# Kernel optimization log

Hardware: AMD Instinct MI355X
Metric: run time of the kernel (lower is better)

Reference implementation:

```python
import jax, jax.numpy as jnp
import numpy as np

N_USERS = 1_000_000
AVG_DEG = 32
E = N_USERS * AVG_DEG
K = 5
IN_F = 1
OUT_F = 64
BN_EPS = 1e-5


def setup_inputs() -> dict:
    key = jax.random.key(0)
    ks = jax.random.split(key, 6)
    stdv = 1.0 / np.sqrt(IN_F * K)
    return {
        "x": jax.random.normal(ks[0], (N_USERS, IN_F), dtype=jnp.float32),
        "edge_index": jax.random.randint(ks[1], (2, E), 0, N_USERS, dtype=jnp.int32),
        "edge_weight": jax.random.uniform(ks[2], (E,), dtype=jnp.float32),
        "weight": jax.random.uniform(ks[3], (OUT_F, K, IN_F), dtype=jnp.float32, minval=-stdv, maxval=stdv),
        "bias": jax.random.uniform(ks[4], (OUT_F,), dtype=jnp.float32, minval=-stdv, maxval=stdv),
        "gamma": jnp.ones((N_USERS,), dtype=jnp.float32),
        "beta": jnp.zeros((N_USERS,), dtype=jnp.float32),
    }


def reference(x, edge_index, edge_weight, weight, bias, gamma, beta):
    N = x.shape[0]
    src, dst = edge_index[0], edge_index[1]
    # K-hop propagation: gather x_j, scale by edge_weight, scatter-add at dst
    feats = [x]
    cur = x
    for _ in range(K - 1):
        msg = cur[src] * edge_weight[:, None]                 # [E, IN_F]
        cur = jax.ops.segment_sum(msg, dst, num_segments=N)   # [N, IN_F]
        feats.append(cur)
    # [N, K*IN_F], hop-major / feature-minor ordering (matches torch reshape)
    conv = jnp.concatenate(feats, axis=1)[None]               # [1, N, K*IN_F]
    h = weight.reshape(OUT_F, K * IN_F).T                     # [K*IN_F, OUT_F]
    y = jnp.matmul(conv, h) + bias                            # [1, N, OUT_F]
    # BatchNorm1d(N_users) in training mode: stats over (batch, feature) per node-channel
    mean = jnp.mean(y, axis=(0, 2), keepdims=True)
    var = jnp.mean((y - mean) ** 2, axis=(0, 2), keepdims=True)  # biased var
    y_hat = (y - mean) * jax.lax.rsqrt(var + BN_EPS)
    return y_hat * gamma[None, :, None] + beta[None, :, None]
```

## Files before the change

### kernel.cpp

```cpp
#include <hip/hip_runtime.h>

#define N_USERS 1000000
#define NEDGE   32000000
#define OUT_F   64
#define BN_EPS  1e-5f

#define SBITS     12
#define S_BUCKET  4096
#define NB        245
#define CAP       136896
#define SCAT_BLOCKS 1024
#define TILE      4096
#define NTILES    ((NEDGE + TILE - 1) / TILE)
#define SPLIT     8

typedef unsigned int uint4v __attribute__((ext_vector_type(4)));


__global__ void init_cursors(unsigned* __restrict__ cursors) {
    int i = blockIdx.x * blockDim.x + threadIdx.x;
    if (i < NB) cursors[i] = (unsigned)i * CAP;
}

__global__ __launch_bounds__(256) void scatter_bin(
    const int* __restrict__ src, const int* __restrict__ dst,
    const float* __restrict__ ew, uint2* __restrict__ rec,
    unsigned* __restrict__ cursors) {
    __shared__ uint2 srec[TILE];
    __shared__ unsigned short sbkt[TILE];
    __shared__ unsigned hist[NB];
    __shared__ unsigned curs[NB];
    __shared__ unsigned gpos[NB];
    int tid = threadIdx.x;

    for (int tile = blockIdx.x; tile < NTILES; tile += gridDim.x) {
        int e0 = tile * TILE;
        int n_this = (e0 + TILE <= NEDGE) ? TILE : (NEDGE - e0);

        for (int i = tid; i < NB; i += 256) hist[i] = 0;
        __syncthreads();

        int d[16];
        #pragma unroll
        for (int k = 0; k < 16; ++k) {
            int e = e0 + k * 256 + tid;
            if (e < NEDGE) {
                d[k] = __builtin_nontemporal_load(&dst[e]);
                atomicAdd(&hist[d[k] >> SBITS], 1u);
            }
        }
        __syncthreads();

        if (tid == 0) {
            unsigned run = 0;
            for (int b = 0; b < NB; ++b) { unsigned v = hist[b]; hist[b] = run; run += v; }
        }
        __syncthreads();

        for (int b = tid; b < NB; b += 256) {
            unsigned st = hist[b];
            unsigned en = (b == NB - 1) ? (unsigned)n_this : hist[b + 1];
            unsigned c = en - st;
            gpos[b] = c ? atomicAdd(&cursors[b], c) : 0u;
            curs[b] = 0;
        }
        __syncthreads();

        #pragma unroll
        for (int k = 0; k < 16; ++k) {
            int e = e0 + k * 256 + tid;
            if (e < NEDGE) {
                int dd = d[k];
                int b = dd >> SBITS;
                int s = __builtin_nontemporal_load(&src[e]);
                float w = __builtin_nontemporal_load(&ew[e]);
                unsigned p = hist[b] + atomicAdd(&curs[b], 1u);
                srec[p] = make_uint2(((unsigned)(dd & (S_BUCKET - 1)) << 20) | (unsigned)s,
                                     __float_as_uint(w));
                sbkt[p] = (unsigned short)b;
            }
        }
        __syncthreads();

        for (int i = tid; i < n_this; i += 256) {
            unsigned b = sbkt[i];
            rec[gpos[b] + ((unsigned)i - hist[b])] = srec[i];
        }
        __syncthreads();
    }
}

__global__ __launch_bounds__(256) void hop_bucket(
    const uint2* __restrict__ rec, const unsigned* __restrict__ cursors,
    const float* __restrict__ cur, float* __restrict__ nxt) {
    __shared__ float acc[S_BUCKET];
    int tid = threadIdx.x;
    int b = blockIdx.x / SPLIT;
    int sidx = blockIdx.x % SPLIT;
    for (int i = tid; i < S_BUCKET; i += 256) acc[i] = 0.0f;
    __syncthreads();

    unsigned start = (unsigned)b * CAP;
    unsigned cnt = cursors[b] - start;
    unsigned u0 = ((cnt * (unsigned)sidx) / SPLIT) & ~3u;
    unsigned u1 = (sidx == SPLIT - 1) ? cnt : (((cnt * (unsigned)(sidx + 1)) / SPLIT) & ~3u);
    const uint2* bp = rec + start;

    unsigned i = u0 + 4u * (unsigned)tid;
    for (; i + 4u <= u1; i += 4u * 256u) {
        uint4v r0 = __builtin_nontemporal_load(reinterpret_cast<const uint4v*>(bp + i));
        uint4v r1 = __builtin_nontemporal_load(reinterpret_cast<const uint4v*>(bp + i + 2));
        float c0 = cur[r0.x & 0xFFFFFu];
        float c1 = cur[r0.z & 0xFFFFFu];
        float c2 = cur[r1.x & 0xFFFFFu];
        float c3 = cur[r1.z & 0xFFFFFu];
        atomicAdd(&acc[r0.x >> 20], c0 * __uint_as_float(r0.y));
        atomicAdd(&acc[r0.z >> 20], c1 * __uint_as_float(r0.w));
        atomicAdd(&acc[r1.x >> 20], c2 * __uint_as_float(r1.y));
        atomicAdd(&acc[r1.z >> 20], c3 * __uint_as_float(r1.w));
    }
    if (i < u1) {
        for (unsigned j = i; j < i + 4u && j < u1; ++j) {
            uint2 r = bp[j];
            atomicAdd(&acc[r.x >> 20], cur[r.x & 0xFFFFFu] * __uint_as_float(r.y));
        }
    }
    __syncthreads();

    int nb0 = b << SBITS;
    for (int k = tid; k < S_BUCKET; k += 256) {
        int n = nb0 + k;
        if (n < N_USERS) atomicAdd(&nxt[n], acc[k]);
    }
}


__global__ void zero_kernel(float* __restrict__ p, int n) {
    int i = blockIdx.x * blockDim.x + threadIdx.x;
    int stride = gridDim.x * blockDim.x;
    for (; i < n; i += stride) p[i] = 0.0f;
}

__global__ __launch_bounds__(256) void hop_atomic(
    const int* __restrict__ src, const int* __restrict__ dst,
    const float* __restrict__ ew, const float* __restrict__ cur,
    float* __restrict__ nxt) {
    int e = blockIdx.x * blockDim.x + threadIdx.x;
    if (e * 4 < NEDGE) {
        int4   s = ((const int4*)src)[e];
        int4   d = ((const int4*)dst)[e];
        float4 w = ((const float4*)ew)[e];
        atomicAdd(&nxt[d.x], cur[s.x] * w.x);
        atomicAdd(&nxt[d.y], cur[s.y] * w.y);
        atomicAdd(&nxt[d.z], cur[s.z] * w.z);
        atomicAdd(&nxt[d.w], cur[s.w] * w.w);
    }
}


__global__ __launch_bounds__(256) void finalize_kernel(
    const float* __restrict__ x,  const float* __restrict__ f1,
    const float* __restrict__ f2, const float* __restrict__ f3,
    const float* __restrict__ f4, const float* __restrict__ W,
    const float* __restrict__ bias, const float* __restrict__ gamma,
    const float* __restrict__ beta, float* __restrict__ out) {
    int lane = threadIdx.x & 63;
    int waveInBlock = threadIdx.x >> 6;
    int wavesPerBlock = blockDim.x >> 6;
    int gwave  = blockIdx.x * wavesPerBlock + waveInBlock;
    int nwaves = gridDim.x * wavesPerBlock;

    float w0 = W[lane * 5 + 0];
    float w1 = W[lane * 5 + 1];
    float w2 = W[lane * 5 + 2];
    float w3 = W[lane * 5 + 3];
    float w4 = W[lane * 5 + 4];
    float b  = bias[lane];

    for (int n = gwave; n < N_USERS; n += nwaves) {
        float c0 = x[n], c1 = f1[n], c2 = f2[n], c3 = f3[n], c4 = f4[n];
        float y = b + c0 * w0 + c1 * w1 + c2 * w2 + c3 * w3 + c4 * w4;

        float s = y;
        #pragma unroll
        for (int off = 32; off; off >>= 1) s += __shfl_xor(s, off);
        float mean = s * (1.0f / 64.0f);

        float d = y - mean;
        float v = d * d;
        #pragma unroll
        for (int off = 32; off; off >>= 1) v += __shfl_xor(v, off);
        float var = v * (1.0f / 64.0f);

        float o = d * rsqrtf(var + BN_EPS) * gamma[n] + beta[n];
        __builtin_nontemporal_store(o, &out[(size_t)n * OUT_F + lane]);
    }
}

extern "C" void kernel_launch(void* const* d_in, const int* in_sizes, int n_in,
                              void* d_out, int out_size, void* d_ws, size_t ws_size,
                              hipStream_t stream) {
    const float* x     = (const float*)d_in[0];
    const int*   ei    = (const int*)d_in[1];
    const float* ew    = (const float*)d_in[2];
    const float* W     = (const float*)d_in[3];
    const float* bias  = (const float*)d_in[4];
    const float* gamma = (const float*)d_in[5];
    const float* beta  = (const float*)d_in[6];
    float* out = (float*)d_out;

    const int* src = ei;
    const int* dst = ei + NEDGE;

    float* f = (float*)d_ws;
    uint2* rec = (uint2*)(f + 4ull * N_USERS);
    unsigned* cursors = (unsigned*)(rec + (size_t)NB * CAP);
    size_t needed = 16000000ull + (size_t)NB * CAP * 8 + 4096;

    if (ws_size >= needed) {
        init_cursors<<<1, 256, 0, stream>>>(cursors);
        zero_kernel<<<2048, 256, 0, stream>>>(f, 4 * N_USERS);
        scatter_bin<<<SCAT_BLOCKS, 256, 0, stream>>>(src, dst, ew, rec, cursors);
        const float* cur = x;
        for (int h = 0; h < 4; ++h) {
            float* nxt = f + (size_t)h * N_USERS;
            hop_bucket<<<NB * SPLIT, 256, 0, stream>>>(rec, cursors, cur, nxt);
            cur = nxt;
        }
    } else {
        zero_kernel<<<4096, 256, 0, stream>>>(f, 4 * N_USERS);
        const float* cur = x;
        for (int h = 0; h < 4; ++h) {
            float* nxt = f + (size_t)h * N_USERS;
            hop_atomic<<<NEDGE / 4 / 256, 256, 0, stream>>>(src, dst, ew, cur, nxt);
            cur = nxt;
        }
    }

    finalize_kernel<<<2048, 256, 0, stream>>>(
        x, f, f + N_USERS, f + 2 * N_USERS, f + 3 * N_USERS,
        W, bias, gamma, beta, out);
}
```

Before: 1.781 ms.

## Sub-bin destination buckets by source quarter to localize gathers

Each destination bucket is split into four sub-bins by which quarter of the source-node range the edge reads from. Each hop block then walks the sub-bins in order, so at any moment the blocks gather from a narrower slice of the feature array, aiming for better L2 locality. The serial prefix scan in the binning kernel becomes a two-level parallel scan to cope with four times as many bins. Costs include more global cursors and atomics, more load imbalance because the per-bin capacity is tighter, and more loop overhead per hop block.

```diff
diff --git a/kernel.cpp b/kernel.cpp
--- a/kernel.cpp
+++ b/kernel.cpp
@@ -8,7 +8,10 @@
 #define SBITS     12
 #define S_BUCKET  4096
 #define NB        245
-#define CAP       136896
+#define KSRC      4
+#define QW        250000
+#define NBINS     (NB * KSRC)
+#define CAP_BIN   34832
 #define SCAT_BLOCKS 1024
 #define TILE      4096
 #define NTILES    ((NEDGE + TILE - 1) / TILE)
@@ -16,10 +19,14 @@
 
 typedef unsigned int uint4v __attribute__((ext_vector_type(4)));
 
+__device__ __forceinline__ int src_quarter(unsigned s) {
+    return (s >= 1u * QW) + (s >= 2u * QW) + (s >= 3u * QW);
+}
+
 
 __global__ void init_cursors(unsigned* __restrict__ cursors) {
     int i = blockIdx.x * blockDim.x + threadIdx.x;
-    if (i < NB) cursors[i] = (unsigned)i * CAP;
+    if (i < NBINS) cursors[i] = (unsigned)i * CAP_BIN;
 }
 
 __global__ __launch_bounds__(256) void scatter_bin(
@@ -28,41 +35,67 @@
     unsigned* __restrict__ cursors) {
     __shared__ uint2 srec[TILE];
     __shared__ unsigned short sbkt[TILE];
-    __shared__ unsigned hist[NB];
-    __shared__ unsigned curs[NB];
-    __shared__ unsigned gpos[NB];
+    __shared__ unsigned hist[NBINS];
+    __shared__ unsigned curs[NBINS];
+    __shared__ unsigned gpos[NBINS];
+    __shared__ unsigned chunkT[256];
     int tid = threadIdx.x;
 
     for (int tile = blockIdx.x; tile < NTILES; tile += gridDim.x) {
         int e0 = tile * TILE;
         int n_this = (e0 + TILE <= NEDGE) ? TILE : (NEDGE - e0);
 
-        for (int i = tid; i < NB; i += 256) hist[i] = 0;
-        __syncthreads();
-
-        int d[16];
+        for (int i = tid; i < NBINS; i += 256) hist[i] = 0;
+        __syncthreads();
+
+        int dv[16], sv[16];
         #pragma unroll
         for (int k = 0; k < 16; ++k) {
             int e = e0 + k * 256 + tid;
             if (e < NEDGE) {
-                d[k] = __builtin_nontemporal_load(&dst[e]);
-                atomicAdd(&hist[d[k] >> SBITS], 1u);
-            }
-        }
-        __syncthreads();
-
+                dv[k] = __builtin_nontemporal_load(&dst[e]);
+                sv[k] = __builtin_nontemporal_load(&src[e]);
+                int bin = ((dv[k] >> SBITS) << 2) | src_quarter((unsigned)sv[k]);
+                atomicAdd(&hist[bin], 1u);
+            }
+        }
+        __syncthreads();
+
+        {
+            int base = tid * 4;
+            unsigned run = 0;
+            #pragma unroll
+            for (int k = 0; k < 4; ++k) {
+                int idx = base + k;
+                unsigned v = (idx < NBINS) ? hist[idx] : 0u;
+                if (idx < NBINS) hist[idx] = run;
+                run += v;
+            }
+            chunkT[tid] = run;
+        }
+        __syncthreads();
         if (tid == 0) {
-            unsigned run = 0;
-            for (int b = 0; b < NB; ++b) { unsigned v = hist[b]; hist[b] = run; run += v; }
-        }
-        __syncthreads();
-
-        for (int b = tid; b < NB; b += 256) {
-            unsigned st = hist[b];
-            unsigned en = (b == NB - 1) ? (unsigned)n_this : hist[b + 1];
+            unsigned r = 0;
+            for (int t = 0; t < 256; ++t) { unsigned v = chunkT[t]; chunkT[t] = r; r += v; }
+        }
+        __syncthreads();
+        {
+            int base = tid * 4;
+            unsigned add = chunkT[tid];
+            #pragma unroll
+            for (int k = 0; k < 4; ++k) {
+                int idx = base + k;
+                if (idx < NBINS) hist[idx] += add;
+            }
+        }
+        __syncthreads();
+
+        for (int bn = tid; bn < NBINS; bn += 256) {
+            unsigned st = hist[bn];
+            unsigned en = (bn == NBINS - 1) ? (unsigned)n_this : hist[bn + 1];
             unsigned c = en - st;
-            gpos[b] = c ? atomicAdd(&cursors[b], c) : 0u;
-            curs[b] = 0;
+            gpos[bn] = c ? atomicAdd(&cursors[bn], c) : 0u;
+            curs[bn] = 0;
         }
         __syncthreads();
 
@@ -70,21 +103,20 @@
         for (int k = 0; k < 16; ++k) {
             int e = e0 + k * 256 + tid;
             if (e < NEDGE) {
-                int dd = d[k];
-                int b = dd >> SBITS;
-                int s = __builtin_nontemporal_load(&src[e]);
+                int dd = dv[k], ss = sv[k];
+                int bin = ((dd >> SBITS) << 2) | src_quarter((unsigned)ss);
                 float w = __builtin_nontemporal_load(&ew[e]);
-                unsigned p = hist[b] + atomicAdd(&curs[b], 1u);
-                srec[p] = make_uint2(((unsigned)(dd & (S_BUCKET - 1)) << 20) | (unsigned)s,
+                unsigned p = hist[bin] + atomicAdd(&curs[bin], 1u);
+                srec[p] = make_uint2(((unsigned)(dd & (S_BUCKET - 1)) << 20) | (unsigned)ss,
                                      __float_as_uint(w));
-                sbkt[p] = (unsigned short)b;
+                sbkt[p] = (unsigned short)bin;
             }
         }
         __syncthreads();
 
         for (int i = tid; i < n_this; i += 256) {
-            unsigned b = sbkt[i];
-            rec[gpos[b] + ((unsigned)i - hist[b])] = srec[i];
+            unsigned bn = sbkt[i];
+            rec[gpos[bn] + ((unsigned)i - hist[bn])] = srec[i];
         }
         __syncthreads();
     }
@@ -100,29 +132,32 @@
     for (int i = tid; i < S_BUCKET; i += 256) acc[i] = 0.0f;
     __syncthreads();
 
-    unsigned start = (unsigned)b * CAP;
-    unsigned cnt = cursors[b] - start;
-    unsigned u0 = ((cnt * (unsigned)sidx) / SPLIT) & ~3u;
-    unsigned u1 = (sidx == SPLIT - 1) ? cnt : (((cnt * (unsigned)(sidx + 1)) / SPLIT) & ~3u);
-    const uint2* bp = rec + start;
-
-    unsigned i = u0 + 4u * (unsigned)tid;
-    for (; i + 4u <= u1; i += 4u * 256u) {
-        uint4v r0 = __builtin_nontemporal_load(reinterpret_cast<const uint4v*>(bp + i));
-        uint4v r1 = __builtin_nontemporal_load(reinterpret_cast<const uint4v*>(bp + i + 2));
-        float c0 = cur[r0.x & 0xFFFFFu];
-        float c1 = cur[r0.z & 0xFFFFFu];
-        float c2 = cur[r1.x & 0xFFFFFu];
-        float c3 = cur[r1.z & 0xFFFFFu];
-        atomicAdd(&acc[r0.x >> 20], c0 * __uint_as_float(r0.y));
-        atomicAdd(&acc[r0.z >> 20], c1 * __uint_as_float(r0.w));
-        atomicAdd(&acc[r1.x >> 20], c2 * __uint_as_float(r1.y));
-        atomicAdd(&acc[r1.z >> 20], c3 * __uint_as_float(r1.w));
-    }
-    if (i < u1) {
-        for (unsigned j = i; j < i + 4u && j < u1; ++j) {
-            uint2 r = bp[j];
-            atomicAdd(&acc[r.x >> 20], cur[r.x & 0xFFFFFu] * __uint_as_float(r.y));
+    for (int k = 0; k < KSRC; ++k) {
+        int bin = b * KSRC + k;
+        unsigned start = (unsigned)bin * CAP_BIN;
+        unsigned cnt = cursors[bin] - start;
+        unsigned u0 = ((cnt * (unsigned)sidx) / SPLIT) & ~3u;
+        unsigned u1 = (sidx == SPLIT - 1) ? cnt : (((cnt * (unsigned)(sidx + 1)) / SPLIT) & ~3u);
+        const uint2* bp = rec + start;
+
+        unsigned i = u0 + 4u * (unsigned)tid;
+        for (; i + 4u <= u1; i += 4u * 256u) {
+            uint4v r0 = __builtin_nontemporal_load(reinterpret_cast<const uint4v*>(bp + i));
+            uint4v r1 = __builtin_nontemporal_load(reinterpret_cast<const uint4v*>(bp + i + 2));
+            float c0 = cur[r0.x & 0xFFFFFu];
+            float c1 = cur[r0.z & 0xFFFFFu];
+            float c2 = cur[r1.x & 0xFFFFFu];
+            float c3 = cur[r1.z & 0xFFFFFu];
+            atomicAdd(&acc[r0.x >> 20], c0 * __uint_as_float(r0.y));
+            atomicAdd(&acc[r0.z >> 20], c1 * __uint_as_float(r0.w));
+            atomicAdd(&acc[r1.x >> 20], c2 * __uint_as_float(r1.y));
+            atomicAdd(&acc[r1.z >> 20], c3 * __uint_as_float(r1.w));
+        }
+        if (i < u1) {
+            for (unsigned j = i; j < i + 4u && j < u1; ++j) {
+                uint2 r = bp[j];
+                atomicAdd(&acc[r.x >> 20], cur[r.x & 0xFFFFFu] * __uint_as_float(r.y));
+            }
         }
     }
     __syncthreads();
@@ -214,11 +249,11 @@
 
     float* f = (float*)d_ws;
     uint2* rec = (uint2*)(f + 4ull * N_USERS);
-    unsigned* cursors = (unsigned*)(rec + (size_t)NB * CAP);
-    size_t needed = 16000000ull + (size_t)NB * CAP * 8 + 4096;
+    unsigned* cursors = (unsigned*)(rec + (size_t)NBINS * CAP_BIN);
+    size_t needed = 16000000ull + (size_t)NBINS * CAP_BIN * 8 + 4096;
 
     if (ws_size >= needed) {
-        init_cursors<<<1, 256, 0, stream>>>(cursors);
+        init_cursors<<<(NBINS + 255) / 256, 256, 0, stream>>>(cursors);
         zero_kernel<<<2048, 256, 0, stream>>>(f, 4 * N_USERS);
         scatter_bin<<<SCAT_BLOCKS, 256, 0, stream>>>(src, dst, ew, rec, cursors);
         const float* cur = x;
```

After: 1.810 ms. About the same (+1.6%).
